# Kernel optimization log

Hardware: AMD Instinct MI355X
Metric: run time of the kernel (lower is better)

The kernel has to match this reference:

```python
import jax, jax.numpy as jnp
import numpy as np

ALPHA = 1.0
BETA = 10.0
OHEM_RATIO = 3
EPS = 1e-7  # clamp for BCE logs (torch BCELoss clamps log at -100; EPS keeps it finite)


def setup_inputs() -> dict:
    key = jax.random.key(0)
    k1, k2, k3, k4 = jax.random.split(key, 4)
    B, H, W = 16, 640, 640
    # channel 0 is a probability map (fed to BCELoss directly) -> uniform (0,1)
    outputs = jax.random.uniform(k1, (B, 3, H, W), dtype=jnp.float32)
    gt_shrink_labels = jax.random.bernoulli(k2, 0.05, (B, H, W)).astype(jnp.float32)
    # border threshold map in [0,1], mostly zero
    gt_threshold_labels = (jax.random.uniform(k3, (B, H, W), dtype=jnp.float32)
                           * jax.random.bernoulli(k4, 0.1, (B, H, W)).astype(jnp.float32))
    return {
        "outputs": outputs,
        "gt_shrink_labels": gt_shrink_labels,
        "gt_threshold_labels": gt_threshold_labels,
    }


def _ohem_mask(score, gt):
    """Per-sample OHEM: keep all positives + top (pos_num*ratio) hardest negatives.
    score, gt: [H, W]. Returns float mask [H, W]. Mirrors ohem_single exactly."""
    n = score.size
    pos = gt > 0.5
    pos_num = jnp.sum(pos)
    neg_cnt = n - pos_num
    neg_num = jnp.minimum(pos_num * OHEM_RATIO, neg_cnt)
    # negatives only, sorted descending (positives pushed to the bottom)
    neg_scores = jnp.where(pos.ravel(), -jnp.inf, score.ravel())
    sorted_desc = -jnp.sort(-neg_scores)
    idx = jnp.clip(neg_num - 1, 0, n - 1)
    thr = sorted_desc[idx]
    sel = ((score >= thr) | pos).astype(score.dtype)
    all_ones = (pos_num == 0) | (neg_num == 0)
    return jnp.where(all_ones, jnp.ones_like(score), sel)


def _masked_bce(p, t, m):
    """Mean BCE over masked pixels (= torch BCELoss on the selected subset)."""
    p = jnp.clip(p, EPS, 1.0 - EPS)
    l = -(t * jnp.log(p) + (1.0 - t) * jnp.log1p(-p))
    s = jnp.sum(m)
    return jnp.where(s > 0, jnp.sum(l * m) / jnp.maximum(s, 1.0), 0.0)


def _bce_loss(prob, gt):
    mask = jax.lax.stop_gradient(_ohem_mask(prob, gt))  # torch uses .data (detached)
    return _masked_bce(prob, gt, mask)


def _threshold_loss(thr_map, gt_thr, gt_shrink):
    sel = ((gt_thr > 0) | (gt_shrink > 0)).astype(thr_map.dtype)
    s = jnp.sum(sel)
    l1 = jnp.sum(jnp.abs(thr_map - gt_thr) * sel)
    return jnp.where(s > 0, l1 / jnp.maximum(s, 1.0), 0.0)


def _per_sample(shrink_map, threshold_map, binary_map, gt_shrink, gt_thr):
    loss_shrink = _bce_loss(shrink_map, gt_shrink)
    loss_binary = _bce_loss(jax.nn.sigmoid(binary_map), gt_shrink)
    loss_threshold = _threshold_loss(threshold_map, gt_thr, gt_shrink)
    return loss_shrink, loss_binary, loss_threshold


def reference(outputs, gt_shrink_labels, gt_threshold_labels):
    shrink_maps = outputs[:, 0, :, :]
    threshold_maps = outputs[:, 1, :, :]
    binary_maps = outputs[:, 2, :, :]
    ls, lb, lt = jax.vmap(_per_sample)(shrink_maps, threshold_maps, binary_maps,
                                       gt_shrink_labels, gt_threshold_labels)
    # reduction == 'mean'
    loss_shrink = jnp.mean(ls)
    loss_binary = jnp.mean(lb)
    loss_threshold = jnp.mean(lt)
    loss_all = loss_shrink + ALPHA * loss_binary + BETA * loss_threshold
    return (loss_all, loss_shrink, loss_binary, loss_threshold)
```

## Files before the change

### kernel.cpp

```cpp
#include <hip/hip_runtime.h>
#include <math.h>
#include <stddef.h>

#define BATCH 16
#define NPIX (640 * 640)
#define NBIN 512
#define FIXS 4096.0f

struct WS {
  float posNum[BATCH];
  float posLossS[BATCH];
  float posLossB[BATCH];
  float selCnt[BATCH];
  float l1Sum[BATCH];
  float lsPart[BATCH];
  float lbPart[BATCH];
  unsigned long long hist[2][BATCH][NBIN];
};

__device__ __forceinline__ int bucketOf(float x) {
  int b = (int)(x * (float)NBIN);
  return b < 0 ? 0 : (b > NBIN - 1 ? NBIN - 1 : b);
}

__device__ __forceinline__ float blockSum(float v, volatile float* lds4) {
#pragma unroll
  for (int o = 32; o > 0; o >>= 1) v += __shfl_down(v, o, 64);
  int lane = threadIdx.x & 63, w = threadIdx.x >> 6;
  __syncthreads();
  if (lane == 0) lds4[w] = v;
  __syncthreads();
  return lds4[0] + lds4[1] + lds4[2] + lds4[3];
}

__global__ void __launch_bounds__(256) k_main(const float* __restrict__ out4,
                                              const float* __restrict__ gts,
                                              const float* __restrict__ gtt,
                                              WS* ws) {
  const int s = blockIdx.y;
  __shared__ unsigned long long h0[NBIN], h1[NBIN];
  for (int i = threadIdx.x; i < NBIN; i += 256) { h0[i] = 0ull; h1[i] = 0ull; }
  __syncthreads();

  const float4* p0 = (const float4*)(out4 + ((size_t)s * 3 + 0) * NPIX);
  const float4* p1 = (const float4*)(out4 + ((size_t)s * 3 + 1) * NPIX);
  const float4* p2 = (const float4*)(out4 + ((size_t)s * 3 + 2) * NPIX);
  const float4* g = (const float4*)(gts + (size_t)s * NPIX);
  const float4* t = (const float4*)(gtt + (size_t)s * NPIX);
  const int n4 = NPIX / 4;
  const float lo = 1e-7f, hi = 1.0f - 1e-7f;

  float posC = 0.f, pls = 0.f, plb = 0.f, sel = 0.f, l1 = 0.f;

  auto proc = [&](const float4& gv, const float4& tv, const float4& a1,
                  const float4& a0, const float4& a2) {
    float ga[4] = {gv.x, gv.y, gv.z, gv.w};
    float ta[4] = {tv.x, tv.y, tv.z, tv.w};
    float y1[4] = {a1.x, a1.y, a1.z, a1.w};
    float y0[4] = {a0.x, a0.y, a0.z, a0.w};
    float y2[4] = {a2.x, a2.y, a2.z, a2.w};
#pragma unroll
    for (int j = 0; j < 4; ++j) {
      const float tt = ga[j];
      const bool posp = tt > 0.5f;
      if (ta[j] > 0.f || tt > 0.f) {
        sel += 1.f;
        l1 += fabsf(y1[j] - ta[j]);
      }
      const float p = fminf(fmaxf(y0[j], lo), hi);
      const float l0 = -__logf(posp ? p : 1.f - p);
      const float xb = y2[j];
      const float l2 = __logf(1.f + __expf(posp ? -xb : xb));
      if (posp) {
        posC += 1.f; pls += l0; plb += l2;
      } else {
        unsigned long long pk0 =
            (1ull << 32) | (unsigned long long)__float2uint_rn(l0 * FIXS);
        unsigned long long pk1 =
            (1ull << 32) | (unsigned long long)__float2uint_rn(l2 * FIXS);
        atomicAdd(&h0[bucketOf(y0[j])], pk0);
        atomicAdd(&h1[bucketOf(xb)], pk1);
      }
    }
  };

  const int stride = gridDim.x * 256;
  int i = blockIdx.x * 256 + threadIdx.x;
  if (i < n4) {
    float4 gv = g[i], tv = t[i], a1 = p1[i], a0 = p0[i], a2 = p2[i];
    for (;;) {
      const int nx = i + stride;
      if (nx < n4) {
        float4 gv2 = g[nx], tv2 = t[nx], b1 = p1[nx], b0 = p0[nx], b2 = p2[nx];
        proc(gv, tv, a1, a0, a2);
        gv = gv2; tv = tv2; a1 = b1; a0 = b0; a2 = b2;
        i = nx;
      } else {
        proc(gv, tv, a1, a0, a2);
        break;
      }
    }
  }
  __syncthreads();

  for (int b = threadIdx.x; b < NBIN; b += 256) {
    unsigned long long v = h0[b];
    if (v) atomicAdd(&ws->hist[0][s][b], v);
    v = h1[b];
    if (v) atomicAdd(&ws->hist[1][s][b], v);
  }

  __shared__ float lds4[4];
  float r;
  r = blockSum(posC, lds4);
  if (threadIdx.x == 0) atomicAdd(&ws->posNum[s], r);
  r = blockSum(pls, lds4);
  if (threadIdx.x == 0) atomicAdd(&ws->posLossS[s], r);
  r = blockSum(plb, lds4);
  if (threadIdx.x == 0) atomicAdd(&ws->posLossB[s], r);
  r = blockSum(sel, lds4);
  if (threadIdx.x == 0) atomicAdd(&ws->selCnt[s], r);
  r = blockSum(l1, lds4);
  if (threadIdx.x == 0) atomicAdd(&ws->l1Sum[s], r);
}

__global__ void __launch_bounds__(256) k_fin(WS* ws) {
  const int ty = blockIdx.x, s = blockIdx.y;
  const int tid = threadIdx.x;
  __shared__ float sc[256], sl[256];
  __shared__ float meanS;

  const unsigned long long* hh = ws->hist[ty][s];
  const float pos = ws->posNum[s];
  const float posLoss = ty ? ws->posLossB[s] : ws->posLossS[s];
  const float negc = (float)NPIX - pos;
  const float k = fminf(3.f * pos, negc);

  const int base = tid * 2;
  const unsigned long long v0 = hh[base], v1 = hh[base + 1];
  const float c0 = (float)(unsigned)(v0 >> 32);
  const float c1 = (float)(unsigned)(v1 >> 32);
  const float s0 = (float)(unsigned)(v0 & 0xffffffffu) * (1.0f / FIXS);
  const float s1 = (float)(unsigned)(v1 & 0xffffffffu) * (1.0f / FIXS);
  sc[tid] = c0 + c1;
  sl[tid] = s0 + s1;
  __syncthreads();
  for (int off = 1; off < 256; off <<= 1) {
    float ac = (tid + off < 256) ? sc[tid + off] : 0.f;
    float al = (tid + off < 256) ? sl[tid + off] : 0.f;
    __syncthreads();
    sc[tid] += ac;
    sl[tid] += al;
    __syncthreads();
  }
  if (k < 0.5f) {
    if (tid == 0) meanS = (posLoss + sl[0]) / (float)NPIX;
  } else {
    const float cumT = sc[tid];
    const float cumN = (tid < 255) ? sc[tid + 1] : 0.f;
    const float slN = (tid < 255) ? sl[tid + 1] : 0.f;
    if (cumT >= k && cumN < k) {
      float C_above, nb, bsum, S_above;
      if (cumN + c1 >= k) {
        C_above = cumN; nb = c1; bsum = s1; S_above = slN;
      } else {
        C_above = cumN + c1; nb = c0; bsum = s0; S_above = slN + s1;
      }
      const float krem = k - C_above;
      const float maskCnt = pos + C_above + krem;
      const float lossSum = posLoss + S_above + bsum * (krem / nb);
      meanS = lossSum / fmaxf(maskCnt, 1.f);
    }
  }
  __syncthreads();
  if (tid == 0) {
    if (ty) ws->lbPart[s] = meanS;
    else    ws->lsPart[s] = meanS;
  }
}

__global__ void k_out(const WS* __restrict__ ws, float* __restrict__ out) {
  if (threadIdx.x == 0) {
    float ls = 0.f, lb = 0.f, lt = 0.f;
    for (int s = 0; s < BATCH; ++s) {
      ls += ws->lsPart[s];
      lb += ws->lbPart[s];
      float sc = ws->selCnt[s];
      lt += (sc > 0.f) ? ws->l1Sum[s] / fmaxf(sc, 1.f) : 0.f;
    }
    ls /= (float)BATCH;
    lb /= (float)BATCH;
    lt /= (float)BATCH;
    out[0] = ls + 1.0f * lb + 10.0f * lt;
    out[1] = ls;
    out[2] = lb;
    out[3] = lt;
  }
}

extern "C" void kernel_launch(void* const* d_in, const int* in_sizes, int n_in,
                              void* d_out, int out_size, void* d_ws,
                              size_t ws_size, hipStream_t stream) {
  const float* out4 = (const float*)d_in[0];
  const float* gts = (const float*)d_in[1];
  const float* gtt = (const float*)d_in[2];
  WS* ws = (WS*)d_ws;

  hipMemsetAsync(d_ws, 0, sizeof(WS), stream);

  k_main<<<dim3(128, BATCH), dim3(256), 0, stream>>>(out4, gts, gtt, ws);
  k_fin<<<dim3(2, BATCH), dim3(256), 0, stream>>>(ws);
  k_out<<<1, 64, 0, stream>>>(ws, (float*)d_out);
}
```

Baseline: 200.0 us.

## Spread global histogram atomics over slots, fuse final reduction into k_fin

Global histograms are split into 8 slots per sample so blocks merging their shared-memory histograms contend less on the same global addresses, and k_fin sums the slots. The separate k_out launch is removed: the last finishing k_fin block, found with a done counter, computes the final outputs. The main grid is halved to 64 blocks per sample with an occupancy hint in launch_bounds, and a scheduling barrier keeps next-iteration loads ahead of the compute. This trades a larger workspace to memset and more per-block work for fewer global atomic conflicts and one fewer launch.

```diff
diff --git a/kernel.cpp b/kernel.cpp
--- a/kernel.cpp
+++ b/kernel.cpp
@@ -5,6 +5,7 @@
 #define BATCH 16
 #define NPIX (640 * 640)
 #define NBIN 512
+#define NSLOT 8
 #define FIXS 4096.0f
 
 struct WS {
@@ -15,7 +16,8 @@
   float l1Sum[BATCH];
   float lsPart[BATCH];
   float lbPart[BATCH];
-  unsigned long long hist[2][BATCH][NBIN];
+  unsigned doneCnt;
+  unsigned long long hist[2][BATCH][NSLOT][NBIN];
 };
 
 __device__ __forceinline__ int bucketOf(float x) {
@@ -33,11 +35,12 @@
   return lds4[0] + lds4[1] + lds4[2] + lds4[3];
 }
 
-__global__ void __launch_bounds__(256) k_main(const float* __restrict__ out4,
-                                              const float* __restrict__ gts,
-                                              const float* __restrict__ gtt,
-                                              WS* ws) {
+__global__ void __launch_bounds__(256, 4) k_main(const float* __restrict__ out4,
+                                                 const float* __restrict__ gts,
+                                                 const float* __restrict__ gtt,
+                                                 WS* ws) {
   const int s = blockIdx.y;
+  const int slot = blockIdx.x & (NSLOT - 1);
   __shared__ unsigned long long h0[NBIN], h1[NBIN];
   for (int i = threadIdx.x; i < NBIN; i += 256) { h0[i] = 0ull; h1[i] = 0ull; }
   __syncthreads();
@@ -74,12 +77,12 @@
       if (posp) {
         posC += 1.f; pls += l0; plb += l2;
       } else {
-        unsigned long long pk0 =
-            (1ull << 32) | (unsigned long long)__float2uint_rn(l0 * FIXS);
-        unsigned long long pk1 =
-            (1ull << 32) | (unsigned long long)__float2uint_rn(l2 * FIXS);
-        atomicAdd(&h0[bucketOf(y0[j])], pk0);
-        atomicAdd(&h1[bucketOf(xb)], pk1);
+        const int b0 = bucketOf(y0[j]);
+        const int b1 = bucketOf(xb);
+        atomicAdd(&h0[b0],
+                  (1ull << 32) | (unsigned long long)__float2uint_rn(l0 * FIXS));
+        atomicAdd(&h1[b1],
+                  (1ull << 32) | (unsigned long long)__float2uint_rn(l2 * FIXS));
       }
     }
   };
@@ -92,6 +95,7 @@
       const int nx = i + stride;
       if (nx < n4) {
         float4 gv2 = g[nx], tv2 = t[nx], b1 = p1[nx], b0 = p0[nx], b2 = p2[nx];
+        __builtin_amdgcn_sched_barrier(0);
         proc(gv, tv, a1, a0, a2);
         gv = gv2; tv = tv2; a1 = b1; a0 = b0; a2 = b2;
         i = nx;
@@ -105,9 +109,9 @@
 
   for (int b = threadIdx.x; b < NBIN; b += 256) {
     unsigned long long v = h0[b];
-    if (v) atomicAdd(&ws->hist[0][s][b], v);
+    if (v) atomicAdd(&ws->hist[0][s][slot][b], v);
     v = h1[b];
-    if (v) atomicAdd(&ws->hist[1][s][b], v);
+    if (v) atomicAdd(&ws->hist[1][s][slot][b], v);
   }
 
   __shared__ float lds4[4];
@@ -124,24 +128,30 @@
   if (threadIdx.x == 0) atomicAdd(&ws->l1Sum[s], r);
 }
 
-__global__ void __launch_bounds__(256) k_fin(WS* ws) {
+__global__ void __launch_bounds__(256) k_fin(WS* ws, float* __restrict__ out) {
   const int ty = blockIdx.x, s = blockIdx.y;
   const int tid = threadIdx.x;
   __shared__ float sc[256], sl[256];
   __shared__ float meanS;
 
-  const unsigned long long* hh = ws->hist[ty][s];
+  const unsigned long long(*hh)[NBIN] = ws->hist[ty][s];
   const float pos = ws->posNum[s];
   const float posLoss = ty ? ws->posLossB[s] : ws->posLossS[s];
   const float negc = (float)NPIX - pos;
   const float k = fminf(3.f * pos, negc);
 
   const int base = tid * 2;
-  const unsigned long long v0 = hh[base], v1 = hh[base + 1];
-  const float c0 = (float)(unsigned)(v0 >> 32);
-  const float c1 = (float)(unsigned)(v1 >> 32);
-  const float s0 = (float)(unsigned)(v0 & 0xffffffffu) * (1.0f / FIXS);
-  const float s1 = (float)(unsigned)(v1 & 0xffffffffu) * (1.0f / FIXS);
+  float c0 = 0.f, c1 = 0.f, s0 = 0.f, s1 = 0.f;
+#pragma unroll
+  for (int sl2 = 0; sl2 < NSLOT; ++sl2) {
+    const unsigned long long v0 = hh[sl2][base], v1 = hh[sl2][base + 1];
+    c0 += (float)(unsigned)(v0 >> 32);
+    c1 += (float)(unsigned)(v1 >> 32);
+    s0 += (float)(unsigned)(v0 & 0xffffffffu);
+    s1 += (float)(unsigned)(v1 & 0xffffffffu);
+  }
+  s0 *= (1.0f / FIXS);
+  s1 *= (1.0f / FIXS);
   sc[tid] = c0 + c1;
   sl[tid] = s0 + s1;
   __syncthreads();
@@ -176,25 +186,27 @@
   if (tid == 0) {
     if (ty) ws->lbPart[s] = meanS;
     else    ws->lsPart[s] = meanS;
-  }
-}
-
-__global__ void k_out(const WS* __restrict__ ws, float* __restrict__ out) {
-  if (threadIdx.x == 0) {
-    float ls = 0.f, lb = 0.f, lt = 0.f;
-    for (int s = 0; s < BATCH; ++s) {
-      ls += ws->lsPart[s];
-      lb += ws->lbPart[s];
-      float sc = ws->selCnt[s];
-      lt += (sc > 0.f) ? ws->l1Sum[s] / fmaxf(sc, 1.f) : 0.f;
-    }
-    ls /= (float)BATCH;
-    lb /= (float)BATCH;
-    lt /= (float)BATCH;
-    out[0] = ls + 1.0f * lb + 10.0f * lt;
-    out[1] = ls;
-    out[2] = lb;
-    out[3] = lt;
+    __threadfence();
+    unsigned done = atomicAdd(&ws->doneCnt, 1u);
+    if (done == 2 * BATCH - 1) {
+      __threadfence();
+      volatile float* lsP = ws->lsPart;
+      volatile float* lbP = ws->lbPart;
+      float ls = 0.f, lb = 0.f, lt = 0.f;
+      for (int ss = 0; ss < BATCH; ++ss) {
+        ls += lsP[ss];
+        lb += lbP[ss];
+        float scv = ws->selCnt[ss];
+        lt += (scv > 0.f) ? ws->l1Sum[ss] / fmaxf(scv, 1.f) : 0.f;
+      }
+      ls /= (float)BATCH;
+      lb /= (float)BATCH;
+      lt /= (float)BATCH;
+      out[0] = ls + 1.0f * lb + 10.0f * lt;
+      out[1] = ls;
+      out[2] = lb;
+      out[3] = lt;
+    }
   }
 }
 
@@ -208,7 +220,6 @@
 
   hipMemsetAsync(d_ws, 0, sizeof(WS), stream);
 
-  k_main<<<dim3(128, BATCH), dim3(256), 0, stream>>>(out4, gts, gtt, ws);
-  k_fin<<<dim3(2, BATCH), dim3(256), 0, stream>>>(ws);
-  k_out<<<1, 64, 0, stream>>>(ws, (float*)d_out);
-}
+  k_main<<<dim3(64, BATCH), dim3(256), 0, stream>>>(out4, gts, gtt, ws);
+  k_fin<<<dim3(2, BATCH), dim3(256), 0, stream>>>(ws, (float*)d_out);
+}
```

Result: faster. 189.5 us (-5.2%).
